# Kernel tuning notes

Hardware: AMD Instinct MI355X
Metric: run time of the kernel (lower is better)

Reference implementation:

```python
import jax, jax.numpy as jnp
import numpy as np
from jax import lax

TEMPERATURE = 0.5
MOMENTUM = 0.9
EPS = 1e-12  # F.normalize eps

B, D, K = 8192, 512, 16384


def _l2norm(x):
    # matches F.normalize(p=2): x / max(||x||, eps)
    n = jnp.sqrt(jnp.sum(x * x, axis=-1, keepdims=True))
    return x / jnp.maximum(n, EPS)


def setup_inputs() -> dict:
    key = jax.random.key(0)
    k1, k2, k3 = jax.random.split(key, 3)
    embeddings = jax.random.normal(k1, (B, D), dtype=jnp.float32)
    cluster_ids = jax.random.randint(k2, (B,), 0, K, dtype=jnp.int64)
    prototypes = jax.random.normal(k3, (K, D), dtype=jnp.float32)
    return {"embeddings": embeddings, "cluster_ids": cluster_ids, "prototypes": prototypes}


def reference(embeddings, cluster_ids, prototypes):
    emb_n = _l2norm(embeddings)            # [B, D]
    proto_n = _l2norm(prototypes)          # [K, D]
    sim = jnp.einsum('bd,kd->bk', emb_n, proto_n) / TEMPERATURE  # [B, K]

    pos = jnp.take_along_axis(sim, cluster_ids[:, None], axis=1)  # [B, 1]
    # mask out the positive column, then stable logsumexp over negatives
    is_pos = jnp.arange(sim.shape[1])[None, :] == cluster_ids[:, None]  # [B, K]
    neg = jnp.where(is_pos, -jnp.inf, sim)
    lse = jax.scipy.special.logsumexp(neg, axis=1, keepdims=True)       # [B, 1]
    loss = jnp.mean(-pos + lse)

    # serial momentum EMA update (order-dependent for duplicate cluster ids)
    def step(protos, xc):
        x, c = xc
        row = MOMENTUM * protos[c] + (1.0 - MOMENTUM) * x
        return protos.at[c].set(row), None

    new_protos, _ = lax.scan(step, prototypes, (embeddings, cluster_ids))
    return loss, new_protos
```

## Files before the change

kernel.cpp:

```cpp
#include <hip/hip_runtime.h>
#include <hip/hip_bf16.h>


#define B_N 8192
#define D_N 512
#define K_N 16384
#define INV_T 2.0f
#define MOM 0.9f

#define BM 128
#define BKF 128
#define BTR 256
#define KSPLIT 4
#define NTILE 16
#define BUFB 32768
#define CAP 64

typedef __attribute__((ext_vector_type(8))) int intx8;
typedef __attribute__((ext_vector_type(4))) float floatx4;

__device__ __forceinline__ void gl_lds16(const void* g, void* lds) {
    __builtin_amdgcn_global_load_lds(
        (const __attribute__((address_space(1))) void*)g,
        (__attribute__((address_space(3))) void*)lds, 16, 0, 0);
}

__device__ __forceinline__ intx8 frag2(const unsigned char* rp, int o0, int o1) {
    intx8 v;
    ((int4*)&v)[0] = *(const int4*)(rp + o0);
    ((int4*)&v)[1] = *(const int4*)(rp + o1);
    return v;
}

__device__ __forceinline__ floatx4 mxfma(intx8 a, intx8 b, floatx4 c) {
    return __builtin_amdgcn_mfma_scale_f32_16x16x128_f8f6f4(a, b, c, 0, 0, 0,
                                                            0x7F7F7F7F, 0, 0x7F7F7F7F);
}

__global__ void norm_kernel(const float* __restrict__ emb, const float* __restrict__ pro,
                            unsigned char* __restrict__ embq, unsigned char* __restrict__ proq,
                            float* __restrict__ rowsum, float* __restrict__ out) {
    if (blockIdx.x < 32) rowsum[blockIdx.x * 256 + threadIdx.x] = 0.0f;
    if (blockIdx.x == 32 && threadIdx.x == 0) out[0] = 0.0f;
    int row = blockIdx.x * 4 + (threadIdx.x >> 6);
    int lane = threadIdx.x & 63;
    const float* x;
    unsigned char* o;
    if (row < B_N) {
        x = emb + (size_t)row * D_N;
        o = embq + (size_t)row * D_N;
    } else {
        x = pro + (size_t)(row - B_N) * D_N;
        o = proq + (size_t)(row - B_N) * D_N;
    }
    const float4* xp = (const float4*)(x + lane * 8);
    float4 v0 = xp[0];
    float4 v1 = xp[1];
    float ss = v0.x * v0.x + v0.y * v0.y + v0.z * v0.z + v0.w * v0.w +
               v1.x * v1.x + v1.y * v1.y + v1.z * v1.z + v1.w * v1.w;
    #pragma unroll
    for (int of = 32; of; of >>= 1) ss += __shfl_xor(ss, of);
    float sc = 16.0f / fmaxf(sqrtf(ss), 1e-12f);
    int w0 = 0, w1 = 0;
    w0 = __builtin_amdgcn_cvt_pk_fp8_f32(v0.x * sc, v0.y * sc, w0, false);
    w0 = __builtin_amdgcn_cvt_pk_fp8_f32(v0.z * sc, v0.w * sc, w0, true);
    w1 = __builtin_amdgcn_cvt_pk_fp8_f32(v1.x * sc, v1.y * sc, w1, false);
    w1 = __builtin_amdgcn_cvt_pk_fp8_f32(v1.z * sc, v1.w * sc, w1, true);
    int2 st = {w0, w1};
    *(int2*)(o + lane * 8) = st;
}

__global__ void pos_kernel(const float* __restrict__ emb, const float* __restrict__ pro,
                           const int* __restrict__ cid, float* __restrict__ rowpos) {
    int b = blockIdx.x * 4 + (threadIdx.x >> 6);
    int lane = threadIdx.x & 63;
    int c = cid[b];
    const float4* ep = (const float4*)(emb + (size_t)b * D_N + lane * 8);
    const float4* pp = (const float4*)(pro + (size_t)c * D_N + lane * 8);
    float4 e0 = ep[0], e1 = ep[1], p0 = pp[0], p1 = pp[1];
    float dp = e0.x * p0.x + e0.y * p0.y + e0.z * p0.z + e0.w * p0.w +
               e1.x * p1.x + e1.y * p1.y + e1.z * p1.z + e1.w * p1.w;
    float ee = e0.x * e0.x + e0.y * e0.y + e0.z * e0.z + e0.w * e0.w +
               e1.x * e1.x + e1.y * e1.y + e1.z * e1.z + e1.w * e1.w;
    float qq = p0.x * p0.x + p0.y * p0.y + p0.z * p0.z + p0.w * p0.w +
               p1.x * p1.x + p1.y * p1.y + p1.z * p1.z + p1.w * p1.w;
    #pragma unroll
    for (int o = 32; o; o >>= 1) {
        dp += __shfl_xor(dp, o);
        ee += __shfl_xor(ee, o);
        qq += __shfl_xor(qq, o);
    }
    if (lane == 0)
        rowpos[b] = INV_T * dp / (fmaxf(sqrtf(ee), 1e-12f) * fmaxf(sqrtf(qq), 1e-12f));
}

#define FSTEP(CH)                                                                     \
    do {                                                                              \
        const int cc = tt * 4 + (CH);                                                 \
        const int bW = bR >= BUFB ? bR - BUFB : bR + 2 * BUFB;                        \
        if (tt < NTILE - 1 || (CH) < 2) {                                             \
                              \
            const unsigned char* s = bS + (size_t)(((cc + 2) >> 2) * BTR) * D_N +     \
                                     ((((CH) + 2) & 3) << 7);                         \
            unsigned char* d = Bs + bW + ldsW;                                        \
            _Pragma("unroll")                                                         \
            for (int p = 0; p < 4; p++)                                               \
                gl_lds16(s + (size_t)p * 64 * D_N, d + p * 8192);                     \
        }                                                                             \
        const unsigned char* rb = Bs + bR + (wn * 64 + lcol) * BKF;                   \
        intx8 bfA0 = frag2(rb + 0 * (16 * BKF), fsw0, fsw1);                          \
        intx8 bfA1 = frag2(rb + 1 * (16 * BKF), fsw0, fsw1);                          \
        __builtin_amdgcn_s_setprio(1);                                                \
        _Pragma("unroll")                                                             \
        for (int i = 0; i < 4; i++) {                                                 \
            acc[i][0] = mxfma(afr[(CH)][i], bfA0, acc[i][0]);                         \
            acc[i][1] = mxfma(afr[(CH)][i], bfA1, acc[i][1]);                         \
        }                                                                             \
        __builtin_amdgcn_s_setprio(0);                                                \
        intx8 bfB0 = frag2(rb + 2 * (16 * BKF), fsw0, fsw1);                          \
        intx8 bfB1 = frag2(rb + 3 * (16 * BKF), fsw0, fsw1);                          \
        __builtin_amdgcn_s_setprio(1);                                                \
        _Pragma("unroll")                                                             \
        for (int i = 0; i < 4; i++) {                                                 \
            acc[i][2] = mxfma(afr[(CH)][i], bfB0, acc[i][2]);                         \
            acc[i][3] = mxfma(afr[(CH)][i], bfB1, acc[i][3]);                         \
        }                                                                             \
        __builtin_amdgcn_s_setprio(0);                                                \
        if ((CH) == 3) {     \
            _Pragma("unroll")                                                         \
            for (int i = 0; i < 4; i++)                                               \
                _Pragma("unroll")                                                     \
                for (int j = 0; j < 4; j++)                                           \
                    _Pragma("unroll")                                                 \
                    for (int r = 0; r < 4; r++) {                                     \
                        rs[i * 4 + r] += __expf(acc[i][j][r] * (INV_T / 256.0f));     \
                        acc[i][j][r] = 0.0f;                                          \
                    }                                                                 \
        }                                                                             \
        if (tt < NTILE - 1 || (CH) < 2)                                               \
            asm volatile("s_waitcnt vmcnt(4)" ::: "memory");                          \
        else                                                                          \
            asm volatile("s_waitcnt vmcnt(0)" ::: "memory");                          \
        __builtin_amdgcn_s_barrier();                                                 \
        bR = bR == 2 * BUFB ? 0 : bR + BUFB;                                          \
    } while (0)

__global__ __launch_bounds__(512, 2) void flash_kernel(const unsigned char* __restrict__ embq,
                                                       const unsigned char* __restrict__ proq,
                                                       float* __restrict__ rowsum_g) {
    __shared__ __align__(16) unsigned char Bs[3 * BUFB];
    const int t = threadIdx.x;
    const int w = t >> 6, lane = t & 63;
    const int quad = lane >> 4, lcol = lane & 15;
    const int wm = w >> 2, wn = w & 3;

    const int wgl = blockIdx.x + (int)gridDim.x * blockIdx.y;
    const int byp = (wgl & 7) >> 1;
    const int bxp = ((wgl >> 3) << 1) + (wgl & 1);
    const int rowBase = bxp * BM;
    const int kb = byp * (K_N / KSPLIT);

    const int fsw0 = (((quad << 1) | 0) ^ (lcol & 7)) << 4;
    const int fsw1 = (((quad << 1) | 1) ^ (lcol & 7)) << 4;
    const int ldsW = w * 1024;

    const unsigned char* bS = proq + (size_t)(kb + w * 8 + (lane >> 3)) * D_N +
                              (((lane & 7) ^ ((lane >> 3) & 7)) << 4);

    floatx4 acc[4][4];
    float rs[16];
    #pragma unroll
    for (int i = 0; i < 4; i++)
        #pragma unroll
        for (int j = 0; j < 4; j++) {
            floatx4 z = {0.0f, 0.0f, 0.0f, 0.0f};
            acc[i][j] = z;
        }
    #pragma unroll
    for (int i = 0; i < 16; i++) rs[i] = 0.0f;

    intx8 afr[4][4];
    {
        const unsigned char* aBase =
            embq + (size_t)(rowBase + wm * 64 + lcol) * D_N + quad * 32;
        #pragma unroll
        for (int ch = 0; ch < 4; ch++)
            #pragma unroll
            for (int i = 0; i < 4; i++) {
                const unsigned char* p = aBase + (size_t)i * (16 * D_N) + (ch << 7);
                ((int4*)&afr[ch][i])[0] = *(const int4*)(p);
                ((int4*)&afr[ch][i])[1] = *(const int4*)(p + 16);
            }
    }
    #pragma unroll
    for (int p = 0; p < 4; p++)
        gl_lds16(bS + (size_t)p * 64 * D_N, Bs + p * 8192 + ldsW);
    #pragma unroll
    for (int p = 0; p < 4; p++)
        gl_lds16(bS + (size_t)p * 64 * D_N + BKF, Bs + BUFB + p * 8192 + ldsW);
    asm volatile("s_waitcnt vmcnt(4)" ::: "memory");
    __builtin_amdgcn_s_barrier();

    int bR = 0;
    for (int tt = 0; tt < NTILE; tt++) {
        FSTEP(0);
        FSTEP(1);
        FSTEP(2);
        FSTEP(3);
    }

    #pragma unroll
    for (int i = 0; i < 16; i++) {
        #pragma unroll
        for (int o = 1; o < 16; o <<= 1) rs[i] += __shfl_xor(rs[i], o);
    }
    if (lcol == 0) {
        #pragma unroll
        for (int i = 0; i < 4; i++)
            #pragma unroll
            for (int r = 0; r < 4; r++)
                atomicAdd(&rowsum_g[rowBase + wm * 64 + i * 16 + quad * 4 + r],
                          rs[i * 4 + r]);
    }
}

__global__ void loss_kernel(const float* __restrict__ rowsum, const float* __restrict__ rowpos,
                            float* __restrict__ out, int* __restrict__ cnt) {
    __shared__ float red[256];
    int t = threadIdx.x;
    int b = blockIdx.x * 256 + t;
    cnt[b * 2] = 0;
    cnt[b * 2 + 1] = 0;
    float p = rowpos[b];
    red[t] = logf(rowsum[b] - __expf(p)) - p;
    __syncthreads();
    for (int o = 128; o; o >>= 1) {
        if (t < o) red[t] += red[t + o];
        __syncthreads();
    }
    if (t == 0) atomicAdd(out, red[0] * (1.0f / (float)B_N));
}

__global__ void ema_count(const int* __restrict__ cid, int* __restrict__ cnt,
                          int* __restrict__ bucket) {
    int b = blockIdx.x * 256 + threadIdx.x;
    int c = cid[b];
    int slot = atomicAdd(&cnt[c], 1);
    if (slot < CAP) bucket[c * CAP + slot] = b;
}

__global__ void ema_apply(const float* __restrict__ emb, const float* __restrict__ pro,
                          const int* __restrict__ cnt, const int* __restrict__ bucket,
                          float* __restrict__ outp) {
    int k = blockIdx.x * 4 + (threadIdx.x >> 6);
    int lane = threadIdx.x & 63;
    int n = cnt[k];
    n = n < CAP ? n : CAP;
    const float4* pp = (const float4*)(pro + (size_t)k * D_N + lane * 8);
    float4 a0 = pp[0], a1 = pp[1];
    int myb = (lane < n) ? bucket[k * CAP + lane] : 0x7fffffff;
    for (int i = 0; i < n; i++) {
        int m = myb;
        #pragma unroll
        for (int o = 1; o < 64; o <<= 1) {
            int v = __shfl_xor(m, o);
            m = v < m ? v : m;
        }
        const float4* ep = (const float4*)(emb + (size_t)m * D_N + lane * 8);
        float4 e0 = ep[0], e1 = ep[1];
        a0.x = MOM * a0.x + (1.0f - MOM) * e0.x;
        a0.y = MOM * a0.y + (1.0f - MOM) * e0.y;
        a0.z = MOM * a0.z + (1.0f - MOM) * e0.z;
        a0.w = MOM * a0.w + (1.0f - MOM) * e0.w;
        a1.x = MOM * a1.x + (1.0f - MOM) * e1.x;
        a1.y = MOM * a1.y + (1.0f - MOM) * e1.y;
        a1.z = MOM * a1.z + (1.0f - MOM) * e1.z;
        a1.w = MOM * a1.w + (1.0f - MOM) * e1.w;
        if (myb == m) myb = 0x7fffffff;
    }
    float4* op = (float4*)(outp + (size_t)k * D_N + lane * 8);
    op[0] = a0;
    op[1] = a1;
}

extern "C" void kernel_launch(void* const* d_in, const int* in_sizes, int n_in,
                              void* d_out, int out_size, void* d_ws, size_t ws_size,
                              hipStream_t stream) {
    const float* emb = (const float*)d_in[0];
    const int* cid = (const int*)d_in[1];
    const float* pro = (const float*)d_in[2];
    float* out = (float*)d_out;

    char* ws = (char*)d_ws;
    unsigned char* embq = (unsigned char*)ws;
    unsigned char* proq = (unsigned char*)(ws + 4194304);
    float* rowsum = (float*)(ws + 12582912);
    float* rowpos = (float*)(ws + 12615680);
    int* cnt = (int*)(ws + 4194304);
    int* bucket = (int*)(ws + 4194304 + 65536);

    norm_kernel<<<(B_N + K_N) / 4, 256, 0, stream>>>(emb, pro, embq, proq, rowsum, out);
    pos_kernel<<<B_N / 4, 256, 0, stream>>>(emb, pro, cid, rowpos);
    flash_kernel<<<dim3(B_N / BM, KSPLIT), 512, 0, stream>>>(embq, proq, rowsum);
    loss_kernel<<<B_N / 256, 256, 0, stream>>>(rowsum, rowpos, out, cnt);
    ema_count<<<B_N / 256, 256, 0, stream>>>(cid, cnt, bucket);
    ema_apply<<<K_N / 4, 256, 0, stream>>>(emb, pro, cnt, bucket, out + 1);
}
```

Baseline: 211.9 us.

## Shrink flash tile to 4 waves, double KSPLIT, use simple double buffer

```diff
diff --git a/kernel.cpp b/kernel.cpp
--- a/kernel.cpp
+++ b/kernel.cpp
@@ -10,10 +10,10 @@
 
 #define BM 128
 #define BKF 128
-#define BTR 256
-#define KSPLIT 4
+#define BTR 128
+#define KSPLIT 8
 #define NTILE 16
-#define BUFB 32768
+#define BUFB 16384
 #define CAP 64
 
 typedef __attribute__((ext_vector_type(8))) int intx8;
@@ -97,17 +97,15 @@
 #define FSTEP(CH)                                                                     \
     do {                                                                              \
         const int cc = tt * 4 + (CH);                                                 \
-        const int bW = bR >= BUFB ? bR - BUFB : bR + 2 * BUFB;                        \
-        if (tt < NTILE - 1 || (CH) < 2) {                                             \
-                              \
-            const unsigned char* s = bS + (size_t)(((cc + 2) >> 2) * BTR) * D_N +     \
-                                     ((((CH) + 2) & 3) << 7);                         \
-            unsigned char* d = Bs + bW + ldsW;                                        \
+        if (cc + 1 < NTILE * 4) {         \
+            const unsigned char* s = bS + (size_t)(((cc + 1) >> 2) * BTR) * D_N +     \
+                                     ((((CH) + 1) & 3) << 7);                         \
+            unsigned char* d = Bs + ((cc + 1) & 1) * BUFB + w * 1024;                 \
             _Pragma("unroll")                                                         \
             for (int p = 0; p < 4; p++)                                               \
-                gl_lds16(s + (size_t)p * 64 * D_N, d + p * 8192);                     \
-        }                                                                             \
-        const unsigned char* rb = Bs + bR + (wn * 64 + lcol) * BKF;                   \
+                gl_lds16(s + (size_t)p * 32 * D_N, d + p * 4096);                     \
+        }                                                                             \
+        const unsigned char* rb = Bs + ((cc)&1) * BUFB + (wn * 64 + lcol) * BKF;      \
         intx8 bfA0 = frag2(rb + 0 * (16 * BKF), fsw0, fsw1);                          \
         intx8 bfA1 = frag2(rb + 1 * (16 * BKF), fsw0, fsw1);                          \
         __builtin_amdgcn_s_setprio(1);                                                \
@@ -137,32 +135,26 @@
                         acc[i][j][r] = 0.0f;                                          \
                     }                                                                 \
         }                                                                             \
-        if (tt < NTILE - 1 || (CH) < 2)                                               \
-            asm volatile("s_waitcnt vmcnt(4)" ::: "memory");                          \
-        else                                                                          \
-            asm volatile("s_waitcnt vmcnt(0)" ::: "memory");                          \
-        __builtin_amdgcn_s_barrier();                                                 \
-        bR = bR == 2 * BUFB ? 0 : bR + BUFB;                                          \
+        __syncthreads();   \
     } while (0)
 
-__global__ __launch_bounds__(512, 2) void flash_kernel(const unsigned char* __restrict__ embq,
+__global__ __launch_bounds__(256, 2) void flash_kernel(const unsigned char* __restrict__ embq,
                                                        const unsigned char* __restrict__ proq,
                                                        float* __restrict__ rowsum_g) {
-    __shared__ __align__(16) unsigned char Bs[3 * BUFB];
+    __shared__ __align__(16) unsigned char Bs[2 * BUFB];
     const int t = threadIdx.x;
     const int w = t >> 6, lane = t & 63;
     const int quad = lane >> 4, lcol = lane & 15;
-    const int wm = w >> 2, wn = w & 3;
-
-    const int wgl = blockIdx.x + (int)gridDim.x * blockIdx.y;
-    const int byp = (wgl & 7) >> 1;
-    const int bxp = ((wgl >> 3) << 1) + (wgl & 1);
+    const int wm = w >> 1, wn = w & 1;
+
+    const int wgl = blockIdx.x;
+    const int ks = wgl & 7;
+    const int bxp = wgl >> 3;
     const int rowBase = bxp * BM;
-    const int kb = byp * (K_N / KSPLIT);
+    const int kb = ks * (K_N / KSPLIT);
 
     const int fsw0 = (((quad << 1) | 0) ^ (lcol & 7)) << 4;
     const int fsw1 = (((quad << 1) | 1) ^ (lcol & 7)) << 4;
-    const int ldsW = w * 1024;
 
     const unsigned char* bS = proq + (size_t)(kb + w * 8 + (lane >> 3)) * D_N +
                               (((lane & 7) ^ ((lane >> 3) & 7)) << 4);
@@ -194,14 +186,9 @@
     }
     #pragma unroll
     for (int p = 0; p < 4; p++)
-        gl_lds16(bS + (size_t)p * 64 * D_N, Bs + p * 8192 + ldsW);
-    #pragma unroll
-    for (int p = 0; p < 4; p++)
-        gl_lds16(bS + (size_t)p * 64 * D_N + BKF, Bs + BUFB + p * 8192 + ldsW);
-    asm volatile("s_waitcnt vmcnt(4)" ::: "memory");
-    __builtin_amdgcn_s_barrier();
-
-    int bR = 0;
+        gl_lds16(bS + (size_t)p * 32 * D_N, Bs + p * 4096 + w * 1024);
+    __syncthreads();
+
     for (int tt = 0; tt < NTILE; tt++) {
         FSTEP(0);
         FSTEP(1);
@@ -301,7 +288,7 @@
 
     norm_kernel<<<(B_N + K_N) / 4, 256, 0, stream>>>(emb, pro, embq, proq, rowsum, out);
     pos_kernel<<<B_N / 4, 256, 0, stream>>>(emb, pro, cid, rowpos);
-    flash_kernel<<<dim3(B_N / BM, KSPLIT), 512, 0, stream>>>(embq, proq, rowsum);
+    flash_kernel<<<dim3(64 * KSPLIT), 256, 0, stream>>>(embq, proq, rowsum);
     loss_kernel<<<B_N / 256, 256, 0, stream>>>(rowsum, rowpos, out, cnt);
     ema_count<<<B_N / 256, 256, 0, stream>>>(cid, cnt, bucket);
     ema_apply<<<K_N / 4, 256, 0, stream>>>(emb, pro, cnt, bucket, out + 1);
```

New measurement: 190.9 us. 9.9% less time.
